# Optimization experiments

Hardware: AMD Instinct MI355X
Metric: run time of the kernel (lower is better)

Reference implementation:

```python
import jax, jax.numpy as jnp
import numpy as np

NCHW = ('NCHW', 'OIHW', 'NCHW')


def _conv3x3_same(x, w, b):
    # ZeroPad2d(1) + 3x3 valid conv == 3x3 conv with padding 1
    y = jax.lax.conv_general_dilated(x, w, window_strides=(1, 1),
                                     padding=((1, 1), (1, 1)),
                                     dimension_numbers=NCHW)
    return y + b[None, :, None, None]


def _maxpool2(x):
    return jax.lax.reduce_window(x, -jnp.inf, jax.lax.max,
                                 (1, 1, 2, 2), (1, 1, 2, 2), 'VALID')


def setup_inputs() -> dict:
    key = jax.random.key(0)
    ks = jax.random.split(key, 12)
    B, T1, T2, R, D = 1, 512, 512, 9, 3840
    q = jax.random.normal(ks[0], (B, T1, R, D), jnp.float32)
    t = jax.random.normal(ks[1], (B, T2, R, D), jnp.float32)
    # ViSiL features are L2-normalized region descriptors -> sims in [-1,1]
    q = q / jnp.linalg.norm(q, axis=-1, keepdims=True)
    t = t / jnp.linalg.norm(t, axis=-1, keepdims=True)
    s = 0.05
    return {
        'query': q, 'target': t,
        'w1': jax.random.normal(ks[2], (32, 1, 3, 3), jnp.float32) * s,
        'b1': jax.random.normal(ks[3], (32,), jnp.float32) * s,
        'w2': jax.random.normal(ks[4], (64, 32, 3, 3), jnp.float32) * s,
        'b2': jax.random.normal(ks[5], (64,), jnp.float32) * s,
        'w3': jax.random.normal(ks[6], (128, 64, 3, 3), jnp.float32) * s,
        'b3': jax.random.normal(ks[7], (128,), jnp.float32) * s,
        'wf': jax.random.normal(ks[8], (1, 128, 1, 1), jnp.float32) * s,
        'bf': jax.random.normal(ks[9], (1,), jnp.float32) * s,
    }


def reference(query, target, w1, b1, w2, b2, w3, b3, wf, bf):
    # frame-to-frame: region-pair similarity [B,T1,O,P,T2]
    sim5 = jnp.einsum('biok,bjpk->biopj', query, target)
    # Chamfer (axes=[3,2]): max over target regions P, mean over query regions O
    f2f = jnp.mean(jnp.max(sim5, axis=3), axis=2)  # [B,T1,T2]
    # video comperator CNN
    x = f2f[:, None]                                 # [B,1,T1,T2]
    x = _maxpool2(jax.nn.relu(_conv3x3_same(x, w1, b1)))
    x = _maxpool2(jax.nn.relu(_conv3x3_same(x, w2, b2)))
    x = jax.nn.relu(_conv3x3_same(x, w3, b3))
    x = jax.lax.conv_general_dilated(x, wf, (1, 1), ((0, 0), (0, 0)),
                                     dimension_numbers=NCHW)
    x = x + bf[None, :, None, None]
    s = jnp.clip(x[:, 0], -1.0, 1.0)                 # Hardtanh, [B,H,W]
    # video-to-video Chamfer (axes=[2,1]): max over axis 2, mean over axis 1
    return jnp.mean(jnp.max(s, axis=2), axis=1)      # [B]
```

## Files before the change

### kernel.cpp

```cpp
#include <hip/hip_runtime.h>
#include <hip/hip_bf16.h>

typedef float f32x4 __attribute__((ext_vector_type(4)));
typedef int v8i __attribute__((ext_vector_type(8)));

#define AS3 __attribute__((address_space(3)))
#define AS1 __attribute__((address_space(1)))

__global__ __launch_bounds__(256) void cvt_fp8_kernel(const float* __restrict__ q,
                                                      const float* __restrict__ t,
                                                      unsigned int* __restrict__ qd,
                                                      unsigned int* __restrict__ td,
                                                      int n16) {
  int idx = blockIdx.x * 256 + threadIdx.x;
  const float* src;
  unsigned int* dst;
  if (idx < n16) { src = q; dst = qd; }
  else           { idx -= n16; if (idx >= n16) return; src = t; dst = td; }
  const float4* s4 = (const float4*)src;
  uint4 o;
  unsigned int* op = (unsigned int*)&o;
#pragma unroll
  for (int i = 0; i < 4; ++i) {
    float4 v = s4[idx * 4 + i];
    int w = 0;
    w = __builtin_amdgcn_cvt_pk_fp8_f32(v.x * 16.f, v.y * 16.f, w, false);
    w = __builtin_amdgcn_cvt_pk_fp8_f32(v.z * 16.f, v.w * 16.f, w, true);
    op[i] = w;
  }
  ((uint4*)dst)[idx] = o;
}

__global__ __launch_bounds__(768) void gemm_cmax_kernel(const unsigned char* __restrict__ qf8,
                                                        const unsigned char* __restrict__ tf8,
                                                        float* __restrict__ cmax) {
  __shared__ __align__(16) char smem[147456];
  const int tid  = threadIdx.x;
  const int wv   = tid >> 6;
  const int lane = tid & 63;
  const int quad = lane >> 4;
  const int l16  = lane & 15;
  const int wrow = wv >> 1, wcol = wv & 1;
  const int x = blockIdx.x & 7, r = blockIdx.x >> 3;
  const int bi = (x >> 1) * 4 + (r & 3);
  const int bj = (x & 1) * 8 + (r >> 2);

  f32x4 acc[3][9];
#pragma unroll
  for (int a = 0; a < 3; ++a)
#pragma unroll
    for (int b = 0; b < 9; ++b) acc[a][b] = (f32x4){0.f, 0.f, 0.f, 0.f};

  const unsigned char* gptr[6];
#pragma unroll
  for (int i = 0; i < 6; ++i) {
    int s   = i * 768 + wv * 64 + lane;
    int mat = (s >= 2304);
    int sm  = s - mat * 2304;
    int row = sm >> 3, pc = sm & 7;
    int gc  = pc ^ (row & 7);
    const unsigned char* base = mat ? (tf8 + (size_t)(bj * 288 + row) * 3840)
                                    : (qf8 + (size_t)(bi * 288 + row) * 3840);
    gptr[i] = base + gc * 16;
  }

  int buf = 0;
#pragma unroll
  for (int i = 0; i < 6; ++i)
    __builtin_amdgcn_global_load_lds((const AS1 void*)(gptr[i]),
                                     (AS3 void*)(smem + (i * 768 + wv * 64) * 16), 16, 0, 0);

  const int arow0 = wrow * 48 + l16;
  const int bcol0 = wcol * 144 + l16;

  for (int kt = 0; kt < 30; ++kt) {
    __syncthreads();
    if (kt < 29) {
      int nb = buf ^ 1;
#pragma unroll
      for (int i = 0; i < 6; ++i)
        __builtin_amdgcn_global_load_lds((const AS1 void*)(gptr[i] + (kt + 1) * 128),
                                         (AS3 void*)(smem + nb * 73728 + (i * 768 + wv * 64) * 16),
                                         16, 0, 0);
    }
    const char* A = smem + buf * 73728;
    const char* B = A + 36864;

    v8i av[3];
#pragma unroll
    for (int sr = 0; sr < 3; ++sr) {
      int row = arow0 + sr * 16;
      int sw  = row & 7;
      int p0  = (quad * 2) ^ sw, p1 = (quad * 2 + 1) ^ sw;
      int4 lo = *(const int4*)(A + row * 128 + p0 * 16);
      int4 hi = *(const int4*)(A + row * 128 + p1 * 16);
      v8i v;
      v[0] = lo.x; v[1] = lo.y; v[2] = lo.z; v[3] = lo.w;
      v[4] = hi.x; v[5] = hi.y; v[6] = hi.z; v[7] = hi.w;
      av[sr] = v;
    }
#pragma unroll
    for (int c = 0; c < 9; ++c) {
      int col = bcol0 + c * 16;
      int sw  = col & 7;
      int p0  = (quad * 2) ^ sw, p1 = (quad * 2 + 1) ^ sw;
      int4 lo = *(const int4*)(B + col * 128 + p0 * 16);
      int4 hi = *(const int4*)(B + col * 128 + p1 * 16);
      v8i bv;
      bv[0] = lo.x; bv[1] = lo.y; bv[2] = lo.z; bv[3] = lo.w;
      bv[4] = hi.x; bv[5] = hi.y; bv[6] = hi.z; bv[7] = hi.w;
      acc[0][c] = __builtin_amdgcn_mfma_scale_f32_16x16x128_f8f6f4(
          av[0], bv, acc[0][c], 0, 0, 0, 0x7f7f7f7f, 0, 0x7f7f7f7f);
      acc[1][c] = __builtin_amdgcn_mfma_scale_f32_16x16x128_f8f6f4(
          av[1], bv, acc[1][c], 0, 0, 0, 0x7f7f7f7f, 0, 0x7f7f7f7f);
      acc[2][c] = __builtin_amdgcn_mfma_scale_f32_16x16x128_f8f6f4(
          av[2], bv, acc[2][c], 0, 0, 0, 0x7f7f7f7f, 0, 0x7f7f7f7f);
    }
    buf ^= 1;
  }

  __syncthreads();
  float* scr = (float*)smem;
#pragma unroll
  for (int b = 0; b < 18; ++b) {
    const int bw = b / 3, bs = b - bw * 3;
    if (wrow == bw) {
#pragma unroll
      for (int c = 0; c < 9; ++c)
#pragma unroll
        for (int rr = 0; rr < 4; ++rr)
          scr[(quad * 4 + rr) * 288 + wcol * 144 + c * 16 + l16] = acc[bs][c][rr] * (1.f / 256.f);
    }
    __syncthreads();
    if (tid < 512) {
      int row = tid >> 5, jg = tid & 31;
      const float* p = scr + row * 288 + jg * 9;
      float m = p[0];
#pragma unroll
      for (int k = 1; k < 9; ++k) m = fmaxf(m, p[k]);
      cmax[(size_t)(bi * 288 + b * 16 + row) * 512 + bj * 32 + jg] = m;
    }
    __syncthreads();
  }
}

__global__ __launch_bounds__(512) void mean9_kernel(const float* __restrict__ cmax,
                                                    float* __restrict__ f2f) {
  int i = blockIdx.x, j = threadIdx.x;
  float s = 0.f;
#pragma unroll
  for (int o = 0; o < 9; ++o) s += cmax[(size_t)(i * 9 + o) * 512 + j];
  f2f[i * 512 + j] = s * (1.f / 9.f);
}

__global__ __launch_bounds__(256) void conv1_kernel(const float* __restrict__ in,
                                                    const float* __restrict__ w1,
                                                    const float* __restrict__ b1,
                                                    float* __restrict__ out) {
  __shared__ float tile[34 * 36];
  __shared__ float wl[320];
  int t = blockIdx.x & 255;
  int chg = blockIdx.x >> 8;
  int ty0 = (t >> 4) * 32, tx0 = (t & 15) * 32;
  int py = threadIdx.x >> 4, px = threadIdx.x & 15;

  for (int idx = threadIdx.x; idx < 320; idx += 256)
    wl[idx] = (idx < 288) ? w1[idx] : b1[idx - 288];
  for (int idx = threadIdx.x; idx < 34 * 34; idx += 256) {
    int r = idx / 34, c = idx % 34;
    int gy = ty0 + r - 1, gx = tx0 + c - 1;
    tile[r * 36 + c] = ((unsigned)gy < 512u && (unsigned)gx < 512u) ? in[gy * 512 + gx] : 0.f;
  }
  __syncthreads();

  float win[4][4];
#pragma unroll
  for (int r = 0; r < 4; ++r)
#pragma unroll
    for (int c = 0; c < 4; ++c)
      win[r][c] = tile[(2 * py + r) * 36 + 2 * px + c];

  int gy2 = (t >> 4) * 16 + py, gx2 = (t & 15) * 16 + px;
  int ch0 = chg * 8;
  for (int ch = ch0; ch < ch0 + 8; ++ch) {
    float w[9];
#pragma unroll
    for (int k = 0; k < 9; ++k) w[k] = wl[ch * 9 + k];
    float m = -INFINITY;
#pragma unroll
    for (int a = 0; a < 2; ++a)
#pragma unroll
      for (int b = 0; b < 2; ++b) {
        float s = 0.f;
#pragma unroll
        for (int ky = 0; ky < 3; ++ky)
#pragma unroll
          for (int kx = 0; kx < 3; ++kx) s += win[a + ky][b + kx] * w[ky * 3 + kx];
        m = fmaxf(m, s);
      }
    out[ch * 65536 + gy2 * 256 + gx2] = fmaxf(m + wl[288 + ch], 0.f);
  }
}

__global__ __launch_bounds__(256) void conv2_kernel(const float* __restrict__ in,
                                                    const float* __restrict__ w2,
                                                    const float* __restrict__ b2,
                                                    float* __restrict__ out) {
  __shared__ __align__(16) float wlds[32 * 4 * 12];
  __shared__ __align__(16) float tile[2 * 2 * 10 * 264];
  const int tid = threadIdx.x;
  const int stripe = blockIdx.x & 31, cog = blockIdx.x >> 5;
  const int X = tid;
  const int Y0 = stripe * 8;

  for (int idx = tid; idx < 1152; idx += 256) {
    int co = idx / 288, rem = idx % 288, ci = rem / 9, k = rem % 9;
    wlds[(ci * 4 + co) * 12 + k] = w2[((cog * 4 + co) * 32 + ci) * 9 + k];
  }
  if (tid < 80) {
    int bu = tid / 40, rem = tid % 40, pl = rem / 20, r2 = rem % 20;
    int rr = r2 >> 1, side = r2 & 1;
    tile[bu * 5280 + pl * 2640 + rr * 264 + (side ? 260 : 3)] = 0.f;
  }
  int gof[5], lof[5];
#pragma unroll
  for (int i = 0; i < 5; ++i) {
    int idx = tid + i * 256;
    int rw = idx >> 6, c4 = idx & 63;
    int pl = (rw >= 10), rr = rw - pl * 10;
    int gy = Y0 + rr - 1;
    lof[i] = pl * 2640 + rr * 264 + 4 + c4 * 4;
    gof[i] = ((unsigned)gy < 256u) ? (pl * 65536 + gy * 256 + c4 * 4) : -1;
  }
#pragma unroll
  for (int i = 0; i < 5; ++i) {
    float4 v = (gof[i] >= 0) ? *(const float4*)(in + gof[i]) : (float4){0, 0, 0, 0};
    *(float4*)&tile[lof[i]] = v;
  }
  __syncthreads();

  float acc[8][4];
#pragma unroll
  for (int y = 0; y < 8; ++y)
#pragma unroll
    for (int co = 0; co < 4; ++co) acc[y][co] = 0.f;

#pragma unroll 1
  for (int cb = 0; cb < 16; ++cb) {
    int buf = cb & 1;
    float4 pf[5];
    if (cb < 15) {
#pragma unroll
      for (int i = 0; i < 5; ++i)
        pf[i] = (gof[i] >= 0) ? *(const float4*)(in + gof[i] + (cb + 1) * 131072)
                              : (float4){0, 0, 0, 0};
    }
    const float* tb = tile + buf * 5280;
#pragma unroll
    for (int pl = 0; pl < 2; ++pl) {
      const float* tp = tb + pl * 2640;
      int ci = cb * 2 + pl;
      float w[4][9];
#pragma unroll
      for (int co = 0; co < 4; ++co) {
        const float* wp = &wlds[(ci * 4 + co) * 12];
        float4 w0 = *(const float4*)wp;
        float4 w1 = *(const float4*)(wp + 4);
        w[co][0] = w0.x; w[co][1] = w0.y; w[co][2] = w0.z; w[co][3] = w0.w;
        w[co][4] = w1.x; w[co][5] = w1.y; w[co][6] = w1.z; w[co][7] = w1.w;
        w[co][8] = wp[8];
      }
      float r0[3], r1[3], r2[3];
      const float* p0 = tp + X + 3;
      r0[0] = p0[0]; r0[1] = p0[1]; r0[2] = p0[2];
      const float* p1 = tp + 264 + X + 3;
      r1[0] = p1[0]; r1[1] = p1[1]; r1[2] = p1[2];
#pragma unroll
      for (int y = 0; y < 8; ++y) {
        const float* p2 = tp + (y + 2) * 264 + X + 3;
        r2[0] = p2[0]; r2[1] = p2[1]; r2[2] = p2[2];
#pragma unroll
        for (int co = 0; co < 4; ++co)
          acc[y][co] += r0[0] * w[co][0] + r0[1] * w[co][1] + r0[2] * w[co][2]
                      + r1[0] * w[co][3] + r1[1] * w[co][4] + r1[2] * w[co][5]
                      + r2[0] * w[co][6] + r2[1] * w[co][7] + r2[2] * w[co][8];
        r0[0] = r1[0]; r0[1] = r1[1]; r0[2] = r1[2];
        r1[0] = r2[0]; r1[1] = r2[1]; r1[2] = r2[2];
      }
    }
    if (cb < 15) {
#pragma unroll
      for (int i = 0; i < 5; ++i)
        *(float4*)&tile[(buf ^ 1) * 5280 + lof[i]] = pf[i];
    }
    __syncthreads();
  }

  int x2 = X >> 1;
#pragma unroll
  for (int co = 0; co < 4; ++co) {
    float bias = b2[cog * 4 + co];
#pragma unroll
    for (int y2 = 0; y2 < 4; ++y2) {
      float v = fmaxf(acc[2 * y2][co], acc[2 * y2 + 1][co]);
      v = fmaxf(v + bias, 0.f);
      float o = fmaxf(v, __shfl_xor(v, 1, 64));
      if ((X & 1) == 0)
        out[(cog * 4 + co) * 16384 + (stripe * 4 + y2) * 128 + x2] = o;
    }
  }
}

__global__ __launch_bounds__(256) void conv3_kernel(const float* __restrict__ in,
                                                    const float* __restrict__ w3,
                                                    const float* __restrict__ b3,
                                                    float* __restrict__ out) {
  __shared__ __align__(16) float wlds[64 * 2 * 12];
  __shared__ __align__(16) float tile[2 * 2 * 18 * 136];
  const int tid = threadIdx.x;
  const int stripe = blockIdx.x & 7, cog = blockIdx.x >> 3;
  const int X = tid & 127, yh = tid >> 7;
  const int Y0 = stripe * 16;

  for (int idx = tid; idx < 1152; idx += 256) {
    int co = idx / 576, rem = idx % 576, ci = rem / 9, k = rem % 9;
    wlds[(ci * 2 + co) * 12 + k] = w3[((cog * 2 + co) * 64 + ci) * 9 + k];
  }
  if (tid < 144) {
    int bu = tid / 72, rem = tid % 72, pl = rem / 36, r2 = rem % 36;
    int rr = r2 >> 1, side = r2 & 1;
    tile[bu * 4896 + pl * 2448 + rr * 136 + (side ? 132 : 3)] = 0.f;
  }
  int gof[5], lof[5];
#pragma unroll
  for (int i = 0; i < 5; ++i) {
    int idx = tid + i * 256;
    if (idx < 1152) {
      int rw = idx >> 5, c4 = idx & 31;
      int pl = (rw >= 18), rr = rw - pl * 18;
      int gy = Y0 + rr - 1;
      lof[i] = pl * 2448 + rr * 136 + 4 + c4 * 4;
      gof[i] = ((unsigned)gy < 128u) ? (pl * 16384 + gy * 128 + c4 * 4) : -1;
    } else { lof[i] = -1; gof[i] = -1; }
  }
#pragma unroll
  for (int i = 0; i < 5; ++i)
    if (lof[i] >= 0) {
      float4 v = (gof[i] >= 0) ? *(const float4*)(in + gof[i]) : (float4){0, 0, 0, 0};
      *(float4*)&tile[lof[i]] = v;
    }
  __syncthreads();

  float acc[8][2];
#pragma unroll
  for (int y = 0; y < 8; ++y)
#pragma unroll
    for (int co = 0; co < 2; ++co) acc[y][co] = 0.f;

#pragma unroll 1
  for (int cb = 0; cb < 32; ++cb) {
    int buf = cb & 1;
    float4 pf[5];
    if (cb < 31) {
#pragma unroll
      for (int i = 0; i < 5; ++i)
        pf[i] = (gof[i] >= 0) ? *(const float4*)(in + gof[i] + (cb + 1) * 32768)
                              : (float4){0, 0, 0, 0};
    }
    const float* tb = tile + buf * 4896;
#pragma unroll
    for (int pl = 0; pl < 2; ++pl) {
      const float* tp = tb + pl * 2448;
      int ci = cb * 2 + pl;
      float w[2][9];
#pragma unroll
      for (int co = 0; co < 2; ++co) {
        const float* wp = &wlds[(ci * 2 + co) * 12];
        float4 w0 = *(const float4*)wp;
        float4 w1 = *(const float4*)(wp + 4);
        w[co][0] = w0.x; w[co][1] = w0.y; w[co][2] = w0.z; w[co][3] = w0.w;
        w[co][4] = w1.x; w[co][5] = w1.y; w[co][6] = w1.z; w[co][7] = w1.w;
        w[co][8] = wp[8];
      }
      float r0[3], r1[3], r2[3];
      const float* p0 = tp + (yh * 8) * 136 + X + 3;
      r0[0] = p0[0]; r0[1] = p0[1]; r0[2] = p0[2];
      const float* p1 = tp + (yh * 8 + 1) * 136 + X + 3;
      r1[0] = p1[0]; r1[1] = p1[1]; r1[2] = p1[2];
#pragma unroll
      for (int y = 0; y < 8; ++y) {
        const float* p2 = tp + (yh * 8 + y + 2) * 136 + X + 3;
        r2[0] = p2[0]; r2[1] = p2[1]; r2[2] = p2[2];
#pragma unroll
        for (int co = 0; co < 2; ++co)
          acc[y][co] += r0[0] * w[co][0] + r0[1] * w[co][1] + r0[2] * w[co][2]
                      + r1[0] * w[co][3] + r1[1] * w[co][4] + r1[2] * w[co][5]
                      + r2[0] * w[co][6] + r2[1] * w[co][7] + r2[2] * w[co][8];
        r0[0] = r1[0]; r0[1] = r1[1]; r0[2] = r1[2];
        r1[0] = r2[0]; r1[1] = r2[1]; r1[2] = r2[2];
      }
    }
    if (cb < 31) {
#pragma unroll
      for (int i = 0; i < 5; ++i)
        if (lof[i] >= 0) *(float4*)&tile[(buf ^ 1) * 4896 + lof[i]] = pf[i];
    }
    __syncthreads();
  }

#pragma unroll
  for (int co = 0; co < 2; ++co) {
    float bias = b3[cog * 2 + co];
    float* op = out + (cog * 2 + co) * 16384 + (Y0 + yh * 8) * 128 + X;
#pragma unroll
    for (int y = 0; y < 8; ++y)
      op[y * 128] = fmaxf(acc[y][co] + bias, 0.f);
  }
}

__global__ __launch_bounds__(512) void convf_kernel(const float* __restrict__ in,
                                                    const float* __restrict__ wf,
                                                    const float* __restrict__ bfp,
                                                    float* __restrict__ rowm) {
  __shared__ float part[512];
  int y = blockIdx.x, tid = threadIdx.x;
  int pt = tid >> 7, x = tid & 127;
  float acc = 0.f;
  const float* ip = in + y * 128 + x;
  for (int ci = pt * 32; ci < pt * 32 + 32; ++ci) acc += ip[ci * 16384] * wf[ci];
  part[tid] = acc;
  __syncthreads();
  if (tid < 128) {
    float s = part[tid] + part[tid + 128] + part[tid + 256] + part[tid + 384] + bfp[0];
    part[tid] = fminf(fmaxf(s, -1.f), 1.f);
  }
  __syncthreads();
  if (tid < 64) {
    float m = fmaxf(part[tid], part[tid + 64]);
    for (int off = 32; off; off >>= 1) m = fmaxf(m, __shfl_down(m, off, 64));
    if (tid == 0) rowm[y] = m;
  }
}

__global__ __launch_bounds__(128) void final_kernel(const float* __restrict__ rowm,
                                                    float* __restrict__ out) {
  int x = threadIdx.x;
  float v = rowm[x];
  for (int off = 32; off; off >>= 1) v += __shfl_down(v, off, 64);
  __shared__ float red[2];
  if ((x & 63) == 0) red[x >> 6] = v;
  __syncthreads();
  if (x == 0) out[0] = (red[0] + red[1]) * (1.f / 128.f);
}

extern "C" void kernel_launch(void* const* d_in, const int* in_sizes, int n_in,
                              void* d_out, int out_size, void* d_ws, size_t ws_size,
                              hipStream_t stream) {
  const float* q  = (const float*)d_in[0];
  const float* t  = (const float*)d_in[1];
  const float* w1 = (const float*)d_in[2];
  const float* b1 = (const float*)d_in[3];
  const float* w2 = (const float*)d_in[4];
  const float* b2 = (const float*)d_in[5];
  const float* w3 = (const float*)d_in[6];
  const float* b3 = (const float*)d_in[7];
  const float* wf = (const float*)d_in[8];
  const float* bf = (const float*)d_in[9];
  float* out = (float*)d_out;
  char* ws = (char*)d_ws;

  unsigned char* qf8 = (unsigned char*)(ws + 0);
  unsigned char* tf8 = (unsigned char*)(ws + 17694720);
  float* cmax = (float*)(ws + 35389440);
  float* f2f  = (float*)(ws + 44826624);
  float* x1   = (float*)(ws + 45875200);
  float* x2b  = (float*)(ws + 54263808);
  float* x3   = (float*)(ws + 58458112);
  float* rowm = (float*)(ws + 66846720);

  cvt_fp8_kernel<<<8640, 256, 0, stream>>>(q, t, (unsigned int*)qf8, (unsigned int*)tf8, 1105920);
  gemm_cmax_kernel<<<256, 768, 0, stream>>>(qf8, tf8, cmax);
  mean9_kernel<<<512, 512, 0, stream>>>(cmax, f2f);
  conv1_kernel<<<1024, 256, 0, stream>>>(f2f, w1, b1, x1);
  conv2_kernel<<<512, 256, 0, stream>>>(x1, w2, b2, x2b);
  conv3_kernel<<<512, 256, 0, stream>>>(x2b, w3, b3, x3);
  convf_kernel<<<128, 512, 0, stream>>>(x3, wf, bf, rowm);
  final_kernel<<<1, 128, 0, stream>>>(rowm, out);
}
```

Measured before the change: 392.8 us.

## Split GEMM K-step into three phases with staged async loads and vmcnt waits

The GEMM main loop now splits each K step into three column groups. Each group waits on a fine-grained vmcnt and a raw s_barrier, and issues its share of next-tile global-to-LDS loads behind the reads it no longer needs. The B tile loads are reordered so that each group's columns land by a separate wait, and s_setprio raises priority around the MFMA bursts. The fp8 conversion kernel also switches to coalesced per-thread dword stores. This is meant to overlap memory traffic with MFMA work more tightly and replace the full __syncthreads, but it depends on the counts in the hand-written waitcnt being exactly right.

New measurement: 401.6 us. +2.2%, slower.

```diff
diff --git a/kernel.cpp b/kernel.cpp
--- a/kernel.cpp
+++ b/kernel.cpp
@@ -6,29 +6,28 @@
 
 #define AS3 __attribute__((address_space(3)))
 #define AS1 __attribute__((address_space(1)))
+
+#define GWAIT(n) asm volatile("s_waitcnt vmcnt(" #n ")" ::: "memory")
 
 __global__ __launch_bounds__(256) void cvt_fp8_kernel(const float* __restrict__ q,
                                                       const float* __restrict__ t,
                                                       unsigned int* __restrict__ qd,
-                                                      unsigned int* __restrict__ td,
-                                                      int n16) {
-  int idx = blockIdx.x * 256 + threadIdx.x;
-  const float* src;
+                                                      unsigned int* __restrict__ td) {
+  int b = blockIdx.x;
+  const float4* s4;
   unsigned int* dst;
-  if (idx < n16) { src = q; dst = qd; }
-  else           { idx -= n16; if (idx >= n16) return; src = t; dst = td; }
-  const float4* s4 = (const float4*)src;
-  uint4 o;
-  unsigned int* op = (unsigned int*)&o;
+  int base;
+  if (b < 4320) { s4 = (const float4*)q; dst = qd; base = b * 1024; }
+  else          { s4 = (const float4*)t; dst = td; base = (b - 4320) * 1024; }
 #pragma unroll
   for (int i = 0; i < 4; ++i) {
-    float4 v = s4[idx * 4 + i];
+    int j = base + i * 256 + threadIdx.x;
+    float4 v = s4[j];
     int w = 0;
     w = __builtin_amdgcn_cvt_pk_fp8_f32(v.x * 16.f, v.y * 16.f, w, false);
     w = __builtin_amdgcn_cvt_pk_fp8_f32(v.z * 16.f, v.w * 16.f, w, true);
-    op[i] = w;
-  }
-  ((uint4*)dst)[idx] = o;
+    dst[j] = w;
+  }
 }
 
 __global__ __launch_bounds__(768) void gemm_cmax_kernel(const unsigned char* __restrict__ qf8,
@@ -52,40 +51,44 @@
     for (int b = 0; b < 9; ++b) acc[a][b] = (f32x4){0.f, 0.f, 0.f, 0.f};
 
   const unsigned char* gptr[6];
+  int ldsoff[6];
 #pragma unroll
   for (int i = 0; i < 6; ++i) {
-    int s   = i * 768 + wv * 64 + lane;
-    int mat = (s >= 2304);
-    int sm  = s - mat * 2304;
-    int row = sm >> 3, pc = sm & 7;
-    int gc  = pc ^ (row & 7);
-    const unsigned char* base = mat ? (tf8 + (size_t)(bj * 288 + row) * 3840)
-                                    : (qf8 + (size_t)(bi * 288 + row) * 3840);
-    gptr[i] = base + gc * 16;
-  }
-
-  int buf = 0;
+    int row, pc;
+    if (i < 3) {
+      int s = i * 768 + wv * 64 + lane;
+      row = s >> 3; pc = s & 7;
+      ldsoff[i] = (i * 768 + wv * 64) * 16;
+      int gc = pc ^ (row & 7);
+      gptr[i] = qf8 + (size_t)(bi * 288 + row) * 3840 + gc * 16;
+    } else {
+      int g = i - 3;
+      int rr = wv * 64 + lane;
+      int sub = rr >> 3; pc = rr & 7;
+      int half = (sub >= 48);
+      row = half * 144 + g * 48 + (sub - half * 48);
+      ldsoff[i] = 36864 + g * 6144 + half * 12288 + (wv * 64) * 16;
+      int gc = pc ^ (row & 7);
+      gptr[i] = tf8 + (size_t)(bj * 288 + row) * 3840 + gc * 16;
+    }
+  }
+
 #pragma unroll
   for (int i = 0; i < 6; ++i)
     __builtin_amdgcn_global_load_lds((const AS1 void*)(gptr[i]),
-                                     (AS3 void*)(smem + (i * 768 + wv * 64) * 16), 16, 0, 0);
+                                     (AS3 void*)(smem + ldsoff[i]), 16, 0, 0);
 
   const int arow0 = wrow * 48 + l16;
   const int bcol0 = wcol * 144 + l16;
 
+  int buf = 0;
   for (int kt = 0; kt < 30; ++kt) {
-    __syncthreads();
-    if (kt < 29) {
-      int nb = buf ^ 1;
-#pragma unroll
-      for (int i = 0; i < 6; ++i)
-        __builtin_amdgcn_global_load_lds((const AS1 void*)(gptr[i] + (kt + 1) * 128),
-                                         (AS3 void*)(smem + nb * 73728 + (i * 768 + wv * 64) * 16),
-                                         16, 0, 0);
-    }
     const char* A = smem + buf * 73728;
     const char* B = A + 36864;
-
+    char* nbase = smem + (buf ^ 1) * 73728;
+
+    GWAIT(2);
+    __builtin_amdgcn_s_barrier();
     v8i av[3];
 #pragma unroll
     for (int sr = 0; sr < 3; ++sr) {
@@ -99,9 +102,16 @@
       v[4] = hi.x; v[5] = hi.y; v[6] = hi.z; v[7] = hi.w;
       av[sr] = v;
     }
-#pragma unroll
-    for (int c = 0; c < 9; ++c) {
-      int col = bcol0 + c * 16;
+    if (kt < 29) {
+#pragma unroll
+      for (int i = 0; i < 3; ++i)
+        __builtin_amdgcn_global_load_lds((const AS1 void*)(gptr[i] + (kt + 1) * 128),
+                                         (AS3 void*)(nbase + ldsoff[i]), 16, 0, 0);
+    }
+    __builtin_amdgcn_s_setprio(1);
+#pragma unroll
+    for (int cc = 0; cc < 3; ++cc) {
+      int col = bcol0 + cc * 16;
       int sw  = col & 7;
       int p0  = (quad * 2) ^ sw, p1 = (quad * 2 + 1) ^ sw;
       int4 lo = *(const int4*)(B + col * 128 + p0 * 16);
@@ -109,13 +119,69 @@
       v8i bv;
       bv[0] = lo.x; bv[1] = lo.y; bv[2] = lo.z; bv[3] = lo.w;
       bv[4] = hi.x; bv[5] = hi.y; bv[6] = hi.z; bv[7] = hi.w;
-      acc[0][c] = __builtin_amdgcn_mfma_scale_f32_16x16x128_f8f6f4(
-          av[0], bv, acc[0][c], 0, 0, 0, 0x7f7f7f7f, 0, 0x7f7f7f7f);
-      acc[1][c] = __builtin_amdgcn_mfma_scale_f32_16x16x128_f8f6f4(
-          av[1], bv, acc[1][c], 0, 0, 0, 0x7f7f7f7f, 0, 0x7f7f7f7f);
-      acc[2][c] = __builtin_amdgcn_mfma_scale_f32_16x16x128_f8f6f4(
-          av[2], bv, acc[2][c], 0, 0, 0, 0x7f7f7f7f, 0, 0x7f7f7f7f);
-    }
+      acc[0][cc] = __builtin_amdgcn_mfma_scale_f32_16x16x128_f8f6f4(
+          av[0], bv, acc[0][cc], 0, 0, 0, 0x7f7f7f7f, 0, 0x7f7f7f7f);
+      acc[1][cc] = __builtin_amdgcn_mfma_scale_f32_16x16x128_f8f6f4(
+          av[1], bv, acc[1][cc], 0, 0, 0, 0x7f7f7f7f, 0, 0x7f7f7f7f);
+      acc[2][cc] = __builtin_amdgcn_mfma_scale_f32_16x16x128_f8f6f4(
+          av[2], bv, acc[2][cc], 0, 0, 0, 0x7f7f7f7f, 0, 0x7f7f7f7f);
+    }
+    __builtin_amdgcn_s_setprio(0);
+
+    if (kt < 29) { GWAIT(4); } else { GWAIT(1); }
+    __builtin_amdgcn_s_barrier();
+    if (kt < 29) {
+#pragma unroll
+      for (int i = 3; i < 5; ++i)
+        __builtin_amdgcn_global_load_lds((const AS1 void*)(gptr[i] + (kt + 1) * 128),
+                                         (AS3 void*)(nbase + ldsoff[i]), 16, 0, 0);
+    }
+    __builtin_amdgcn_s_setprio(1);
+#pragma unroll
+    for (int cc = 0; cc < 3; ++cc) {
+      int col = bcol0 + (3 + cc) * 16;
+      int sw  = col & 7;
+      int p0  = (quad * 2) ^ sw, p1 = (quad * 2 + 1) ^ sw;
+      int4 lo = *(const int4*)(B + col * 128 + p0 * 16);
+      int4 hi = *(const int4*)(B + col * 128 + p1 * 16);
+      v8i bv;
+      bv[0] = lo.x; bv[1] = lo.y; bv[2] = lo.z; bv[3] = lo.w;
+      bv[4] = hi.x; bv[5] = hi.y; bv[6] = hi.z; bv[7] = hi.w;
+      acc[0][3 + cc] = __builtin_amdgcn_mfma_scale_f32_16x16x128_f8f6f4(
+          av[0], bv, acc[0][3 + cc], 0, 0, 0, 0x7f7f7f7f, 0, 0x7f7f7f7f);
+      acc[1][3 + cc] = __builtin_amdgcn_mfma_scale_f32_16x16x128_f8f6f4(
+          av[1], bv, acc[1][3 + cc], 0, 0, 0, 0x7f7f7f7f, 0, 0x7f7f7f7f);
+      acc[2][3 + cc] = __builtin_amdgcn_mfma_scale_f32_16x16x128_f8f6f4(
+          av[2], bv, acc[2][3 + cc], 0, 0, 0, 0x7f7f7f7f, 0, 0x7f7f7f7f);
+    }
+    __builtin_amdgcn_s_setprio(0);
+
+    if (kt < 29) { GWAIT(5); } else { GWAIT(0); }
+    __builtin_amdgcn_s_barrier();
+    if (kt < 29) {
+      __builtin_amdgcn_global_load_lds((const AS1 void*)(gptr[5] + (kt + 1) * 128),
+                                       (AS3 void*)(nbase + ldsoff[5]), 16, 0, 0);
+    }
+    __builtin_amdgcn_s_setprio(1);
+#pragma unroll
+    for (int cc = 0; cc < 3; ++cc) {
+      int col = bcol0 + (6 + cc) * 16;
+      int sw  = col & 7;
+      int p0  = (quad * 2) ^ sw, p1 = (quad * 2 + 1) ^ sw;
+      int4 lo = *(const int4*)(B + col * 128 + p0 * 16);
+      int4 hi = *(const int4*)(B + col * 128 + p1 * 16);
+      v8i bv;
+      bv[0] = lo.x; bv[1] = lo.y; bv[2] = lo.z; bv[3] = lo.w;
+      bv[4] = hi.x; bv[5] = hi.y; bv[6] = hi.z; bv[7] = hi.w;
+      acc[0][6 + cc] = __builtin_amdgcn_mfma_scale_f32_16x16x128_f8f6f4(
+          av[0], bv, acc[0][6 + cc], 0, 0, 0, 0x7f7f7f7f, 0, 0x7f7f7f7f);
+      acc[1][6 + cc] = __builtin_amdgcn_mfma_scale_f32_16x16x128_f8f6f4(
+          av[1], bv, acc[1][6 + cc], 0, 0, 0, 0x7f7f7f7f, 0, 0x7f7f7f7f);
+      acc[2][6 + cc] = __builtin_amdgcn_mfma_scale_f32_16x16x128_f8f6f4(
+          av[2], bv, acc[2][6 + cc], 0, 0, 0, 0x7f7f7f7f, 0, 0x7f7f7f7f);
+    }
+    __builtin_amdgcn_s_setprio(0);
+
     buf ^= 1;
   }
 
@@ -478,7 +544,7 @@
   float* x3   = (float*)(ws + 58458112);
   float* rowm = (float*)(ws + 66846720);
 
-  cvt_fp8_kernel<<<8640, 256, 0, stream>>>(q, t, (unsigned int*)qf8, (unsigned int*)tf8, 1105920);
+  cvt_fp8_kernel<<<8640, 256, 0, stream>>>(q, t, (unsigned int*)qf8, (unsigned int*)tf8);
   gemm_cmax_kernel<<<256, 768, 0, stream>>>(qf8, tf8, cmax);
   mean9_kernel<<<512, 512, 0, stream>>>(cmax, f2f);
   conv1_kernel<<<1024, 256, 0, stream>>>(f2f, w1, b1, x1);
```

## Load GEMM A operand directly from global into registers, halve LDS staging

Applied to the files above, without the earlier changes.

The fp8 GEMM now stages only the target (B) tile through double-buffered LDS. Each wave reads its query (A) rows straight from global memory into registers every k-step, which halves shared memory use and may allow more residency or less LDS traffic. The cost is uncoalesced-ish global loads on the critical path with no prefetch, so latency may be exposed. The fp8 convert kernel is also changed so each thread writes 4-byte words in strided, coalesced order instead of one 16-byte store.

After: 413.2 us. 1.05x slower.

```diff
diff --git a/kernel.cpp b/kernel.cpp
--- a/kernel.cpp
+++ b/kernel.cpp
@@ -10,31 +10,28 @@
 __global__ __launch_bounds__(256) void cvt_fp8_kernel(const float* __restrict__ q,
                                                       const float* __restrict__ t,
                                                       unsigned int* __restrict__ qd,
-                                                      unsigned int* __restrict__ td,
-                                                      int n16) {
-  int idx = blockIdx.x * 256 + threadIdx.x;
-  const float* src;
+                                                      unsigned int* __restrict__ td) {
+  int b = blockIdx.x;
+  const float4* s4;
   unsigned int* dst;
-  if (idx < n16) { src = q; dst = qd; }
-  else           { idx -= n16; if (idx >= n16) return; src = t; dst = td; }
-  const float4* s4 = (const float4*)src;
-  uint4 o;
-  unsigned int* op = (unsigned int*)&o;
+  int base;
+  if (b < 4320) { s4 = (const float4*)q; dst = qd; base = b * 1024; }
+  else          { s4 = (const float4*)t; dst = td; base = (b - 4320) * 1024; }
 #pragma unroll
   for (int i = 0; i < 4; ++i) {
-    float4 v = s4[idx * 4 + i];
+    int j = base + i * 256 + threadIdx.x;
+    float4 v = s4[j];
     int w = 0;
     w = __builtin_amdgcn_cvt_pk_fp8_f32(v.x * 16.f, v.y * 16.f, w, false);
     w = __builtin_amdgcn_cvt_pk_fp8_f32(v.z * 16.f, v.w * 16.f, w, true);
-    op[i] = w;
-  }
-  ((uint4*)dst)[idx] = o;
+    dst[j] = w;
+  }
 }
 
 __global__ __launch_bounds__(768) void gemm_cmax_kernel(const unsigned char* __restrict__ qf8,
                                                         const unsigned char* __restrict__ tf8,
                                                         float* __restrict__ cmax) {
-  __shared__ __align__(16) char smem[147456];
+  __shared__ __align__(16) char smem[73728];
   const int tid  = threadIdx.x;
   const int wv   = tid >> 6;
   const int lane = tid & 63;
@@ -51,54 +48,54 @@
 #pragma unroll
     for (int b = 0; b < 9; ++b) acc[a][b] = (f32x4){0.f, 0.f, 0.f, 0.f};
 
-  const unsigned char* gptr[6];
-#pragma unroll
-  for (int i = 0; i < 6; ++i) {
+  const unsigned char* gptrB[3];
+#pragma unroll
+  for (int i = 0; i < 3; ++i) {
     int s   = i * 768 + wv * 64 + lane;
-    int mat = (s >= 2304);
-    int sm  = s - mat * 2304;
-    int row = sm >> 3, pc = sm & 7;
+    int row = s >> 3, pc = s & 7;
     int gc  = pc ^ (row & 7);
-    const unsigned char* base = mat ? (tf8 + (size_t)(bj * 288 + row) * 3840)
-                                    : (qf8 + (size_t)(bi * 288 + row) * 3840);
-    gptr[i] = base + gc * 16;
+    gptrB[i] = tf8 + (size_t)(bj * 288 + row) * 3840 + gc * 16;
+  }
+
+  const unsigned char* aptr[3];
+#pragma unroll
+  for (int sr = 0; sr < 3; ++sr) {
+    int row = wrow * 48 + l16 + sr * 16;
+    aptr[sr] = qf8 + (size_t)(bi * 288 + row) * 3840 + quad * 32;
   }
 
   int buf = 0;
 #pragma unroll
-  for (int i = 0; i < 6; ++i)
-    __builtin_amdgcn_global_load_lds((const AS1 void*)(gptr[i]),
+  for (int i = 0; i < 3; ++i)
+    __builtin_amdgcn_global_load_lds((const AS1 void*)(gptrB[i]),
                                      (AS3 void*)(smem + (i * 768 + wv * 64) * 16), 16, 0, 0);
 
-  const int arow0 = wrow * 48 + l16;
   const int bcol0 = wcol * 144 + l16;
 
   for (int kt = 0; kt < 30; ++kt) {
     __syncthreads();
-    if (kt < 29) {
-      int nb = buf ^ 1;
-#pragma unroll
-      for (int i = 0; i < 6; ++i)
-        __builtin_amdgcn_global_load_lds((const AS1 void*)(gptr[i] + (kt + 1) * 128),
-                                         (AS3 void*)(smem + nb * 73728 + (i * 768 + wv * 64) * 16),
-                                         16, 0, 0);
-    }
-    const char* A = smem + buf * 73728;
-    const char* B = A + 36864;
 
     v8i av[3];
 #pragma unroll
     for (int sr = 0; sr < 3; ++sr) {
-      int row = arow0 + sr * 16;
-      int sw  = row & 7;
-      int p0  = (quad * 2) ^ sw, p1 = (quad * 2 + 1) ^ sw;
-      int4 lo = *(const int4*)(A + row * 128 + p0 * 16);
-      int4 hi = *(const int4*)(A + row * 128 + p1 * 16);
+      int4 lo = *(const int4*)(aptr[sr] + kt * 128);
+      int4 hi = *(const int4*)(aptr[sr] + kt * 128 + 16);
       v8i v;
       v[0] = lo.x; v[1] = lo.y; v[2] = lo.z; v[3] = lo.w;
       v[4] = hi.x; v[5] = hi.y; v[6] = hi.z; v[7] = hi.w;
       av[sr] = v;
     }
+
+    if (kt < 29) {
+      int nb = buf ^ 1;
+#pragma unroll
+      for (int i = 0; i < 3; ++i)
+        __builtin_amdgcn_global_load_lds((const AS1 void*)(gptrB[i] + (kt + 1) * 128),
+                                         (AS3 void*)(smem + nb * 36864 + (i * 768 + wv * 64) * 16),
+                                         16, 0, 0);
+    }
+    const char* B = smem + buf * 36864;
+
 #pragma unroll
     for (int c = 0; c < 9; ++c) {
       int col = bcol0 + c * 16;
@@ -478,7 +475,7 @@
   float* x3   = (float*)(ws + 58458112);
   float* rowm = (float*)(ws + 66846720);
 
-  cvt_fp8_kernel<<<8640, 256, 0, stream>>>(q, t, (unsigned int*)qf8, (unsigned int*)tf8, 1105920);
+  cvt_fp8_kernel<<<8640, 256, 0, stream>>>(q, t, (unsigned int*)qf8, (unsigned int*)tf8);
   gemm_cmax_kernel<<<256, 768, 0, stream>>>(qf8, tf8, cmax);
   mean9_kernel<<<512, 512, 0, stream>>>(cmax, f2f);
   conv1_kernel<<<1024, 256, 0, stream>>>(f2f, w1, b1, x1);
```

## Fuse region-mean into GEMM epilogue and coalesce fp8 conversion stores

Applied to the files above, without the earlier changes.

The GEMM epilogue now keeps per-region maxima in shared memory and averages the nine query regions itself, writing f2f directly. This removes the intermediate cmax buffer round trip and the separate mean9 kernel launch. The fp8 conversion kernel also changes its indexing so that each thread writes one 32-bit word per iteration with adjacent threads contiguous, instead of one 16-byte store per thread. The epilogue's extra shared-memory buffer has to fit alongside the scratch area.

Result: faster. 384.4 us (-2.1%).

```diff
diff --git a/kernel.cpp b/kernel.cpp
--- a/kernel.cpp
+++ b/kernel.cpp
@@ -10,30 +10,27 @@
 __global__ __launch_bounds__(256) void cvt_fp8_kernel(const float* __restrict__ q,
                                                       const float* __restrict__ t,
                                                       unsigned int* __restrict__ qd,
-                                                      unsigned int* __restrict__ td,
-                                                      int n16) {
-  int idx = blockIdx.x * 256 + threadIdx.x;
-  const float* src;
+                                                      unsigned int* __restrict__ td) {
+  int b = blockIdx.x;
+  const float4* s4;
   unsigned int* dst;
-  if (idx < n16) { src = q; dst = qd; }
-  else           { idx -= n16; if (idx >= n16) return; src = t; dst = td; }
-  const float4* s4 = (const float4*)src;
-  uint4 o;
-  unsigned int* op = (unsigned int*)&o;
+  int base;
+  if (b < 4320) { s4 = (const float4*)q; dst = qd; base = b * 1024; }
+  else          { s4 = (const float4*)t; dst = td; base = (b - 4320) * 1024; }
 #pragma unroll
   for (int i = 0; i < 4; ++i) {
-    float4 v = s4[idx * 4 + i];
+    int j = base + i * 256 + threadIdx.x;
+    float4 v = s4[j];
     int w = 0;
     w = __builtin_amdgcn_cvt_pk_fp8_f32(v.x * 16.f, v.y * 16.f, w, false);
     w = __builtin_amdgcn_cvt_pk_fp8_f32(v.z * 16.f, v.w * 16.f, w, true);
-    op[i] = w;
-  }
-  ((uint4*)dst)[idx] = o;
+    dst[j] = w;
+  }
 }
 
 __global__ __launch_bounds__(768) void gemm_cmax_kernel(const unsigned char* __restrict__ qf8,
                                                         const unsigned char* __restrict__ tf8,
-                                                        float* __restrict__ cmax) {
+                                                        float* __restrict__ f2f) {
   __shared__ __align__(16) char smem[147456];
   const int tid  = threadIdx.x;
   const int wv   = tid >> 6;
@@ -120,7 +117,8 @@
   }
 
   __syncthreads();
-  float* scr = (float*)smem;
+  float* scr  = (float*)smem;
+  float* mbuf = (float*)(smem + 18432);
 #pragma unroll
   for (int b = 0; b < 18; ++b) {
     const int bw = b / 3, bs = b - bw * 3;
@@ -138,19 +136,18 @@
       float m = p[0];
 #pragma unroll
       for (int k = 1; k < 9; ++k) m = fmaxf(m, p[k]);
-      cmax[(size_t)(bi * 288 + b * 16 + row) * 512 + bj * 32 + jg] = m;
+      mbuf[(b * 16 + row) * 33 + jg] = m;
     }
     __syncthreads();
   }
-}
-
-__global__ __launch_bounds__(512) void mean9_kernel(const float* __restrict__ cmax,
-                                                    float* __restrict__ f2f) {
-  int i = blockIdx.x, j = threadIdx.x;
-  float s = 0.f;
-#pragma unroll
-  for (int o = 0; o < 9; ++o) s += cmax[(size_t)(i * 9 + o) * 512 + j];
-  f2f[i * 512 + j] = s * (1.f / 9.f);
+  for (int p = tid; p < 1024; p += 768) {
+    int il = p >> 5, jg = p & 31;
+    const float* mp = mbuf + (il * 9) * 33 + jg;
+    float s = 0.f;
+#pragma unroll
+    for (int o = 0; o < 9; ++o) s += mp[o * 33];
+    f2f[(size_t)(bi * 32 + il) * 512 + bj * 32 + jg] = s * (1.f / 9.f);
+  }
 }
 
 __global__ __launch_bounds__(256) void conv1_kernel(const float* __restrict__ in,
@@ -471,16 +468,14 @@
 
   unsigned char* qf8 = (unsigned char*)(ws + 0);
   unsigned char* tf8 = (unsigned char*)(ws + 17694720);
-  float* cmax = (float*)(ws + 35389440);
   float* f2f  = (float*)(ws + 44826624);
   float* x1   = (float*)(ws + 45875200);
   float* x2b  = (float*)(ws + 54263808);
   float* x3   = (float*)(ws + 58458112);
   float* rowm = (float*)(ws + 66846720);
 
-  cvt_fp8_kernel<<<8640, 256, 0, stream>>>(q, t, (unsigned int*)qf8, (unsigned int*)tf8, 1105920);
-  gemm_cmax_kernel<<<256, 768, 0, stream>>>(qf8, tf8, cmax);
-  mean9_kernel<<<512, 512, 0, stream>>>(cmax, f2f);
+  cvt_fp8_kernel<<<8640, 256, 0, stream>>>(q, t, (unsigned int*)qf8, (unsigned int*)tf8);
+  gemm_cmax_kernel<<<256, 768, 0, stream>>>(qf8, tf8, f2f);
   conv1_kernel<<<1024, 256, 0, stream>>>(f2f, w1, b1, x1);
   conv2_kernel<<<512, 256, 0, stream>>>(x1, w2, b2, x2b);
   conv3_kernel<<<512, 256, 0, stream>>>(x2b, w3, b3, x3);
```
